# Performance work log

Measured on AMD Instinct MI355X. Metric: run time of the kernel, lower is better.

Reference implementation:

```python
import jax, jax.numpy as jnp
import numpy as np

T, D, O, E, R = 16384, 4096, 4096, 8, 64  # tokens, in_feat, out_feat, n_adapters, max_rank


def setup_inputs() -> dict:
    key = jax.random.key(0)
    ks = jax.random.split(key, 6)
    x = jax.random.normal(ks[0], (T, D), jnp.float32)
    base_output = jax.random.normal(ks[1], (T, O), jnp.float32)
    A = jax.random.normal(ks[2], (E, D, R), jnp.float32) * 0.02  # loraA per adapter
    B = jax.random.normal(ks[3], (E, R, O), jnp.float32) * 0.02  # loraB per adapter
    scaling = jax.random.uniform(ks[4], (E,), jnp.float32, 0.5, 2.0)  # lora_alpha/rank per adapter
    adapter_ids = jax.random.randint(ks[5], (T,), 0, E, dtype=jnp.int32)  # per-token routing
    return {"x": x, "base_output": base_output, "A": A, "B": B,
            "scaling": scaling, "adapter_ids": adapter_ids}


def reference(x, base_output, A, B, scaling, adapter_ids):
    """S-LoRA batched multi-adapter forward: out = base + (x @ A_i) @ B_i * s_i,
    with adapter i routed per token. Expressed as E masked low-rank GEMMs
    (loop over the small fixed adapter set, vectorized over tokens)."""
    out = base_output
    for e in range(E):
        gate = (adapter_ids == e).astype(x.dtype) * scaling[e]  # (T,)
        h = x @ A[e]                                            # (T, R)
        out = out + (h @ B[e]) * gate[:, None]                  # (T, O)
    return out
```

## Files before the change

kernel.cpp:

```cpp
#include <hip/hip_runtime.h>

#define TT 16384
#define DD 4096
#define OO 4096
#define NE 8
#define RRK 64
#define KSPLIT 4
#define KCHUNK 1024

typedef _Float16 f16x8 __attribute__((ext_vector_type(8)));
typedef float f32x4 __attribute__((ext_vector_type(4)));

#define CNT_OFF 0
#define PERM_OFF 1024
#define AT_OFF (1u << 20)
#define BT_OFF (5u << 20)
#define HP_OFF (9u << 20)

__global__ void prep_kernel(const int* __restrict__ ids,
                            const float* __restrict__ A,
                            const float* __restrict__ B,
                            int* __restrict__ cnt,
                            int* __restrict__ perm,
                            _Float16* __restrict__ At,
                            _Float16* __restrict__ Bt) {
  const int bid = blockIdx.x, tid = threadIdx.x;
  if (bid < 64) {
    int t = bid * 256 + tid;
    int e = ids[t];
    int pos = atomicAdd(&cnt[e], 1);
    perm[e * TT + pos] = t;
    return;
  }
  __shared__ float tile[64][65];
  if (bid < 576) {
    int idx = bid - 64;
    int e = idx >> 6, kb = (idx & 63) << 6;
    #pragma unroll
    for (int i = 0; i < 16; ++i) {
      int lin = i * 256 + tid;
      int kr = lin >> 6, r = lin & 63;
      tile[kr][r] = A[((size_t)e * DD + kb + kr) * RRK + r];
    }
    __syncthreads();
    #pragma unroll
    for (int i = 0; i < 16; ++i) {
      int lin = i * 256 + tid;
      int r = lin >> 6, kk = lin & 63;
      At[((size_t)e * RRK + r) * DD + kb + kk] = (_Float16)tile[kk][r];
    }
  } else {
    int idx = bid - 576;
    int e = idx >> 6, ob = (idx & 63) << 6;
    #pragma unroll
    for (int i = 0; i < 16; ++i) {
      int lin = i * 256 + tid;
      int r = lin >> 6, o = lin & 63;
      tile[r][o] = B[((size_t)e * RRK + r) * OO + ob + o];
    }
    __syncthreads();
    #pragma unroll
    for (int i = 0; i < 16; ++i) {
      int lin = i * 256 + tid;
      int o = lin >> 6, r2 = lin & 63;
      Bt[((size_t)e * OO + ob + o) * RRK + r2] = (_Float16)tile[r2][o];
    }
  }
}

__global__ __launch_bounds__(256, 2)
void lora_stage1(const float* __restrict__ x,
                 const _Float16* __restrict__ At,
                 const int* __restrict__ cnt,
                 const int* __restrict__ perm,
                 _Float16* __restrict__ HP) {
  __shared__ _Float16 Xs[64][72];
  __shared__ _Float16 As[64][72];
  __shared__ int toks[64];
  const int tid = threadIdx.x;
  const int lane = tid & 63, w = tid >> 6;

  int tiles = 0;
  #pragma unroll
  for (int ee = 0; ee < NE; ++ee) tiles += (cnt[ee] + 63) >> 6;

  for (int wi = blockIdx.x; wi < tiles * KSPLIT; wi += gridDim.x) {
    int tile = wi >> 2, s = wi & 3;
    int e = 0, base = 0, n_e = 0;
    {
      int acc0 = 0;
      #pragma unroll
      for (int ee = 0; ee < NE; ++ee) {
        int c = cnt[ee];
        int tl = (c + 63) >> 6;
        if (tile >= acc0 && tile < acc0 + tl) { e = ee; base = acc0; n_e = c; }
        acc0 += tl;
      }
    }
    int m0 = (tile - base) << 6;
    int kbase = s * KCHUNK;

    if (tid < 64) {
      int rloc = m0 + tid;
      toks[tid] = (rloc < n_e) ? perm[e * TT + rloc] : -1;
    }
    __syncthreads();

    const int srow = tid >> 2;
    const int seg = (tid & 3) << 4;
    int tk0 = toks[srow];
    if (tk0 < 0) tk0 = toks[0];
    const float* xp = x + (size_t)tk0 * DD + seg;
    const _Float16* ap = At + ((size_t)e * RRK + srow) * DD + seg;

    f32x4 acc[4] = {};

    for (int k0 = kbase; k0 < kbase + KCHUNK; k0 += 64) {
      float4 v0 = *(const float4*)(xp + k0);
      float4 v1 = *(const float4*)(xp + k0 + 4);
      float4 v2 = *(const float4*)(xp + k0 + 8);
      float4 v3 = *(const float4*)(xp + k0 + 12);
      f16x8 xa, xb;
      xa[0] = (_Float16)v0.x; xa[1] = (_Float16)v0.y;
      xa[2] = (_Float16)v0.z; xa[3] = (_Float16)v0.w;
      xa[4] = (_Float16)v1.x; xa[5] = (_Float16)v1.y;
      xa[6] = (_Float16)v1.z; xa[7] = (_Float16)v1.w;
      xb[0] = (_Float16)v2.x; xb[1] = (_Float16)v2.y;
      xb[2] = (_Float16)v2.z; xb[3] = (_Float16)v2.w;
      xb[4] = (_Float16)v3.x; xb[5] = (_Float16)v3.y;
      xb[6] = (_Float16)v3.z; xb[7] = (_Float16)v3.w;
      *(f16x8*)&Xs[srow][seg] = xa;
      *(f16x8*)&Xs[srow][seg + 8] = xb;
      *(f16x8*)&As[srow][seg] = *(const f16x8*)(ap + k0);
      *(f16x8*)&As[srow][seg + 8] = *(const f16x8*)(ap + k0 + 8);
      __syncthreads();

      const int mr = w * 16 + (lane & 15);
      const int kq = (lane >> 4) << 3;
      #pragma unroll
      for (int ks = 0; ks < 2; ++ks) {
        f16x8 af = *(const f16x8*)&Xs[mr][ks * 32 + kq];
        #pragma unroll
        for (int nf = 0; nf < 4; ++nf) {
          f16x8 bfr = *(const f16x8*)&As[nf * 16 + (lane & 15)][ks * 32 + kq];
          acc[nf] = __builtin_amdgcn_mfma_f32_16x16x32_f16(af, bfr, acc[nf], 0, 0, 0);
        }
      }
      __syncthreads();
    }

    const int rq = (lane >> 4) << 2;
    #pragma unroll
    for (int rg = 0; rg < 4; ++rg) {
      int tk = toks[w * 16 + rq + rg];
      if (tk >= 0) {
        _Float16* hp = HP + ((size_t)s * TT + tk) * RRK + (lane & 15);
        #pragma unroll
        for (int nf = 0; nf < 4; ++nf) {
          hp[nf * 16] = (_Float16)acc[nf][rg];
        }
      }
    }
    __syncthreads();
  }
}

__global__ __launch_bounds__(256, 2)
void lora_stage2(const float* __restrict__ baseo,
                 const _Float16* __restrict__ Bt,
                 const _Float16* __restrict__ HP,
                 const float* __restrict__ scaling,
                 const int* __restrict__ cnt,
                 const int* __restrict__ perm,
                 float* __restrict__ out) {
  __shared__ _Float16 Hs[64][72];
  __shared__ _Float16 Bs[256][72];
  __shared__ int toks[64];
  const int tid = threadIdx.x;
  const int lane = tid & 63, w = tid >> 6;

  int tot = 0;
  #pragma unroll
  for (int ee = 0; ee < NE; ++ee) tot += ((cnt[ee] + 63) >> 6) << 4;

  for (int wi = blockIdx.x; wi < tot; wi += gridDim.x) {
    int e = 0, base = 0, n_e = 0;
    {
      int acc0 = 0;
      #pragma unroll
      for (int ee = 0; ee < NE; ++ee) {
        int c = cnt[ee];
        int tl = ((c + 63) >> 6) << 4;
        if (wi >= acc0 && wi < acc0 + tl) { e = ee; base = acc0; n_e = c; }
        acc0 += tl;
      }
    }
    int local = wi - base;
    int tiles_m = (n_e + 63) >> 6;
    int mt = local % tiles_m;
    int nt = local / tiles_m;
    int m0 = mt << 6, o0 = nt << 8;

    if (tid < 64) {
      int rloc = m0 + tid;
      toks[tid] = (rloc < n_e) ? perm[e * TT + rloc] : -1;
    }
    __syncthreads();

    {
      const f16x8* bp = (const f16x8*)(Bt + ((size_t)e * OO + o0 + tid) * RRK);
      #pragma unroll
      for (int j = 0; j < 8; ++j) *(f16x8*)&Bs[tid][j * 8] = bp[j];
    }
    {
      float s_e = scaling[e];
      int srow = tid >> 2, seg = (tid & 3) << 4;
      int tk = toks[srow];
      if (tk < 0) tk = toks[0];
      float sum[16];
      #pragma unroll
      for (int i = 0; i < 16; ++i) sum[i] = 0.f;
      #pragma unroll
      for (int s = 0; s < KSPLIT; ++s) {
        const f16x8* hp = (const f16x8*)(HP + ((size_t)s * TT + tk) * RRK + seg);
        f16x8 h0 = hp[0], h1 = hp[1];
        #pragma unroll
        for (int i = 0; i < 8; ++i) { sum[i] += (float)h0[i]; sum[8 + i] += (float)h1[i]; }
      }
      f16x8 o0v, o1v;
      #pragma unroll
      for (int i = 0; i < 8; ++i) { o0v[i] = (_Float16)(sum[i] * s_e); o1v[i] = (_Float16)(sum[8 + i] * s_e); }
      *(f16x8*)&Hs[srow][seg] = o0v;
      *(f16x8*)&Hs[srow][seg + 8] = o1v;
    }
    __syncthreads();

    f32x4 acc[16] = {};
    const int kq = (lane >> 4) << 3;
    const int lr = lane & 15;
    #pragma unroll
    for (int ks = 0; ks < 2; ++ks) {
      f16x8 hf = *(const f16x8*)&Hs[w * 16 + lr][ks * 32 + kq];
      #pragma unroll
      for (int of = 0; of < 16; ++of) {
        f16x8 bfr = *(const f16x8*)&Bs[of * 16 + lr][ks * 32 + kq];
        acc[of] = __builtin_amdgcn_mfma_f32_16x16x32_f16(bfr, hf, acc[of], 0, 0, 0);
      }
    }

    int tk = toks[w * 16 + lr];
    if (tk >= 0) {
      const int g4 = (lane >> 4) << 2;
      size_t rowoff = (size_t)tk * OO + o0 + g4;
      #pragma unroll
      for (int of = 0; of < 16; ++of) {
        size_t off = rowoff + of * 16;
        float4 b4 = *(const float4*)(baseo + off);
        float4 r4;
        r4.x = b4.x + acc[of][0];
        r4.y = b4.y + acc[of][1];
        r4.z = b4.z + acc[of][2];
        r4.w = b4.w + acc[of][3];
        *(float4*)(out + off) = r4;
      }
    }
    __syncthreads();
  }
}

extern "C" void kernel_launch(void* const* d_in, const int* in_sizes, int n_in,
                              void* d_out, int out_size, void* d_ws, size_t ws_size,
                              hipStream_t stream) {
  const float* x = (const float*)d_in[0];
  const float* baseo = (const float*)d_in[1];
  const float* A = (const float*)d_in[2];
  const float* B = (const float*)d_in[3];
  const float* scaling = (const float*)d_in[4];
  const int* ids = (const int*)d_in[5];
  float* out = (float*)d_out;
  char* ws = (char*)d_ws;

  int* cnt = (int*)(ws + CNT_OFF);
  int* perm = (int*)(ws + PERM_OFF);
  _Float16* At = (_Float16*)(ws + AT_OFF);
  _Float16* Bt = (_Float16*)(ws + BT_OFF);
  _Float16* HP = (_Float16*)(ws + HP_OFF);

  hipMemsetAsync(cnt, 0, NE * sizeof(int), stream);
  hipLaunchKernelGGL(prep_kernel, dim3(1088), dim3(256), 0, stream,
                     ids, A, B, cnt, perm, At, Bt);
  hipLaunchKernelGGL(lora_stage1, dim3(1056), dim3(256), 0, stream,
                     x, At, cnt, perm, HP);
  hipLaunchKernelGGL(lora_stage2, dim3(4208), dim3(256), 0, stream,
                     baseo, Bt, HP, scaling, cnt, perm, out);
}
```

Measured before the change: 300.4 us.

## Drop LDS staging in LoRA stage2, swizzle blocks, and raise split-K

```diff
diff --git a/kernel.cpp b/kernel.cpp
--- a/kernel.cpp
+++ b/kernel.cpp
@@ -5,10 +5,11 @@
 #define OO 4096
 #define NE 8
 #define RRK 64
-#define KSPLIT 4
-#define KCHUNK 1024
+#define KSPLIT 8
+#define KCHUNK 512
 
 typedef _Float16 f16x8 __attribute__((ext_vector_type(8)));
+typedef _Float16 f16x4 __attribute__((ext_vector_type(4)));
 typedef float f32x4 __attribute__((ext_vector_type(4)));
 
 #define CNT_OFF 0
@@ -68,7 +69,7 @@
   }
 }
 
-__global__ __launch_bounds__(256, 2)
+__global__ __launch_bounds__(256, 4)
 void lora_stage1(const float* __restrict__ x,
                  const _Float16* __restrict__ At,
                  const int* __restrict__ cnt,
@@ -85,7 +86,7 @@
   for (int ee = 0; ee < NE; ++ee) tiles += (cnt[ee] + 63) >> 6;
 
   for (int wi = blockIdx.x; wi < tiles * KSPLIT; wi += gridDim.x) {
-    int tile = wi >> 2, s = wi & 3;
+    int tile = wi >> 3, s = wi & 7;
     int e = 0, base = 0, n_e = 0;
     {
       int acc0 = 0;
@@ -165,7 +166,8 @@
   }
 }
 
-__global__ __launch_bounds__(256, 2)
+#define S2_GRID 4096
+__global__ __launch_bounds__(256, 6)
 void lora_stage2(const float* __restrict__ baseo,
                  const _Float16* __restrict__ Bt,
                  const _Float16* __restrict__ HP,
@@ -173,26 +175,29 @@
                  const int* __restrict__ cnt,
                  const int* __restrict__ perm,
                  float* __restrict__ out) {
-  __shared__ _Float16 Hs[64][72];
-  __shared__ _Float16 Bs[256][72];
-  __shared__ int toks[64];
   const int tid = threadIdx.x;
   const int lane = tid & 63, w = tid >> 6;
+  const int lr = lane & 15;
+  const int g = lane >> 4;
+  const int kq = g << 3;
+  const int g4 = g << 2;
 
   int tot = 0;
   #pragma unroll
   for (int ee = 0; ee < NE; ++ee) tot += ((cnt[ee] + 63) >> 6) << 4;
 
-  for (int wi = blockIdx.x; wi < tot; wi += gridDim.x) {
+  int bs = ((blockIdx.x & 7) << 9) | (blockIdx.x >> 3);
+
+  for (int wi = bs; wi < tot; wi += S2_GRID) {
     int e = 0, base = 0, n_e = 0;
     {
       int acc0 = 0;
       #pragma unroll
       for (int ee = 0; ee < NE; ++ee) {
         int c = cnt[ee];
-        int tl = ((c + 63) >> 6) << 4;
-        if (wi >= acc0 && wi < acc0 + tl) { e = ee; base = acc0; n_e = c; }
-        acc0 += tl;
+        int work = ((c + 63) >> 6) << 4;
+        if (wi >= acc0 && wi < acc0 + work) { e = ee; base = acc0; n_e = c; }
+        acc0 += work;
       }
     }
     int local = wi - base;
@@ -201,60 +206,50 @@
     int nt = local / tiles_m;
     int m0 = mt << 6, o0 = nt << 8;
 
-    if (tid < 64) {
-      int rloc = m0 + tid;
-      toks[tid] = (rloc < n_e) ? perm[e * TT + rloc] : -1;
-    }
-    __syncthreads();
-
+    int row = m0 + w * 16 + lr;
+    bool valid = row < n_e;
+    int tk = perm[e * TT + (valid ? row : n_e - 1)];
+
+    float s_e = scaling[e];
+    f16x8 hf0, hf1;
     {
-      const f16x8* bp = (const f16x8*)(Bt + ((size_t)e * OO + o0 + tid) * RRK);
-      #pragma unroll
-      for (int j = 0; j < 8; ++j) *(f16x8*)&Bs[tid][j * 8] = bp[j];
-    }
-    {
-      float s_e = scaling[e];
-      int srow = tid >> 2, seg = (tid & 3) << 4;
-      int tk = toks[srow];
-      if (tk < 0) tk = toks[0];
       float sum[16];
       #pragma unroll
       for (int i = 0; i < 16; ++i) sum[i] = 0.f;
       #pragma unroll
-      for (int s = 0; s < KSPLIT; ++s) {
-        const f16x8* hp = (const f16x8*)(HP + ((size_t)s * TT + tk) * RRK + seg);
-        f16x8 h0 = hp[0], h1 = hp[1];
+      for (int sp = 0; sp < KSPLIT; ++sp) {
+        const f16x8* hp = (const f16x8*)(HP + ((size_t)sp * TT + tk) * RRK + kq);
+        f16x8 h0 = hp[0];
+        f16x8 h1 = hp[4];
         #pragma unroll
         for (int i = 0; i < 8; ++i) { sum[i] += (float)h0[i]; sum[8 + i] += (float)h1[i]; }
       }
-      f16x8 o0v, o1v;
-      #pragma unroll
-      for (int i = 0; i < 8; ++i) { o0v[i] = (_Float16)(sum[i] * s_e); o1v[i] = (_Float16)(sum[8 + i] * s_e); }
-      *(f16x8*)&Hs[srow][seg] = o0v;
-      *(f16x8*)&Hs[srow][seg + 8] = o1v;
-    }
-    __syncthreads();
-
-    f32x4 acc[16] = {};
-    const int kq = (lane >> 4) << 3;
-    const int lr = lane & 15;
-    #pragma unroll
-    for (int ks = 0; ks < 2; ++ks) {
-      f16x8 hf = *(const f16x8*)&Hs[w * 16 + lr][ks * 32 + kq];
+      #pragma unroll
+      for (int i = 0; i < 8; ++i) {
+        hf0[i] = (_Float16)(sum[i] * s_e);
+        hf1[i] = (_Float16)(sum[8 + i] * s_e);
+      }
+    }
+
+    const _Float16* bp = Bt + ((size_t)e * OO + o0 + lr) * RRK + kq;
+
+    f32x4 acc[16];
+    #pragma unroll
+    for (int of = 0; of < 16; ++of) acc[of] = (f32x4){0.f, 0.f, 0.f, 0.f};
+
+    #pragma unroll
+    for (int of = 0; of < 16; ++of) {
+      f16x8 b0 = *(const f16x8*)(bp + (size_t)of * 16 * RRK);
+      f16x8 b1 = *(const f16x8*)(bp + (size_t)of * 16 * RRK + 32);
+      acc[of] = __builtin_amdgcn_mfma_f32_16x16x32_f16(b0, hf0, acc[of], 0, 0, 0);
+      acc[of] = __builtin_amdgcn_mfma_f32_16x16x32_f16(b1, hf1, acc[of], 0, 0, 0);
+    }
+
+    if (valid) {
+      size_t rowoff = (size_t)tk * OO + o0 + g4;
       #pragma unroll
       for (int of = 0; of < 16; ++of) {
-        f16x8 bfr = *(const f16x8*)&Bs[of * 16 + lr][ks * 32 + kq];
-        acc[of] = __builtin_amdgcn_mfma_f32_16x16x32_f16(bfr, hf, acc[of], 0, 0, 0);
-      }
-    }
-
-    int tk = toks[w * 16 + lr];
-    if (tk >= 0) {
-      const int g4 = (lane >> 4) << 2;
-      size_t rowoff = (size_t)tk * OO + o0 + g4;
-      #pragma unroll
-      for (int of = 0; of < 16; ++of) {
-        size_t off = rowoff + of * 16;
+        size_t off = rowoff + (size_t)of * 16;
         float4 b4 = *(const float4*)(baseo + off);
         float4 r4;
         r4.x = b4.x + acc[of][0];
@@ -264,7 +259,6 @@
         *(float4*)(out + off) = r4;
       }
     }
-    __syncthreads();
   }
 }
 
@@ -289,8 +283,8 @@
   hipMemsetAsync(cnt, 0, NE * sizeof(int), stream);
   hipLaunchKernelGGL(prep_kernel, dim3(1088), dim3(256), 0, stream,
                      ids, A, B, cnt, perm, At, Bt);
-  hipLaunchKernelGGL(lora_stage1, dim3(1056), dim3(256), 0, stream,
+  hipLaunchKernelGGL(lora_stage1, dim3(2048), dim3(256), 0, stream,
                      x, At, cnt, perm, HP);
-  hipLaunchKernelGGL(lora_stage2, dim3(4208), dim3(256), 0, stream,
+  hipLaunchKernelGGL(lora_stage2, dim3(S2_GRID), dim3(256), 0, stream,
                      baseo, Bt, HP, scaling, cnt, perm, out);
 }
```

After: 404.5 us. +34.6%, slower.
